# Optimization experiments

Hardware: AMD Instinct MI355X
Metric: run time of the kernel (lower is better)

Reference implementation:

```python
import jax, jax.numpy as jnp
import numpy as np

B, S, D = 2, 2048, 2048
H = 16
KV_RANK, Q_RANK = 512, 1536
NOPE, ROPE_D, VD = 128, 64, 128
QK_D = NOPE + ROPE_D  # 192


def _rope(t, positions):
    # t: (B, H, S, d) with d even; rotate-half RoPE, theta=10000
    d = t.shape[-1]
    inv_freq = 1.0 / (10000.0 ** (jnp.arange(0, d, 2, dtype=jnp.float32) / d))
    ang = positions.astype(jnp.float32)[:, None] * inv_freq  # (S, d//2)
    cos, sin = jnp.cos(ang), jnp.sin(ang)                    # (S, d//2)
    t1, t2 = t[..., : d // 2], t[..., d // 2 :]
    return jnp.concatenate([t1 * cos - t2 * sin, t2 * cos + t1 * sin], axis=-1)


def setup_inputs() -> dict:
    key = jax.random.key(0)
    ks = jax.random.split(key, 10)
    sc = 0.02
    return {
        "x": jax.random.normal(ks[0], (B, S, D), dtype=jnp.float32),
        "positions": jnp.arange(S, dtype=jnp.int32),
        # torch.nn.Linear weights are (out_features, in_features)
        "Wq_down": jax.random.normal(ks[1], (Q_RANK, D), dtype=jnp.float32) * sc,
        "Wq_up": jax.random.normal(ks[2], (H * NOPE, Q_RANK), dtype=jnp.float32) * sc,
        "Wq_rope": jax.random.normal(ks[3], (H * ROPE_D, Q_RANK), dtype=jnp.float32) * sc,
        "Wkv_down": jax.random.normal(ks[4], (KV_RANK, D), dtype=jnp.float32) * sc,
        "Wk_up": jax.random.normal(ks[5], (H * NOPE, KV_RANK), dtype=jnp.float32) * sc,
        "Wv_up": jax.random.normal(ks[6], (H * VD, KV_RANK), dtype=jnp.float32) * sc,
        "Wk_rope": jax.random.normal(ks[7], (ROPE_D, D), dtype=jnp.float32) * sc,
        "Wo": jax.random.normal(ks[8], (D, H * VD), dtype=jnp.float32) * sc,
    }


def reference(x, positions, Wq_down, Wq_up, Wq_rope, Wkv_down, Wk_up, Wv_up, Wk_rope, Wo):
    bsz, seq_len, _ = x.shape

    # Query path: low-rank down, then nope + rope up-projections
    c_q = x @ Wq_down.T                                             # (B, S, Q_RANK)
    q_c = (c_q @ Wq_up.T).reshape(bsz, seq_len, H, NOPE).transpose(0, 2, 1, 3)
    q_r = (c_q @ Wq_rope.T).reshape(bsz, seq_len, H, ROPE_D).transpose(0, 2, 1, 3)
    q_r = _rope(q_r, positions)
    q = jnp.concatenate([q_c, q_r], axis=-1)                        # (B, H, S, QK_D)

    # KV path: shared latent, single rope head broadcast to all heads
    c_kv = x @ Wkv_down.T                                           # (B, S, KV_RANK)
    k_c = (c_kv @ Wk_up.T).reshape(bsz, seq_len, H, NOPE).transpose(0, 2, 1, 3)
    v_c = (c_kv @ Wv_up.T).reshape(bsz, seq_len, H, VD).transpose(0, 2, 1, 3)
    k_r = (x @ Wk_rope.T).reshape(bsz, seq_len, 1, ROPE_D).transpose(0, 2, 1, 3)
    k_r = _rope(k_r, positions)
    k_r = jnp.broadcast_to(k_r, (bsz, H, seq_len, ROPE_D))
    k = jnp.concatenate([k_c, k_r], axis=-1)                        # (B, H, S, QK_D)

    # Causal SDPA, scale = 1/sqrt(total qk head dim)
    scale = 1.0 / math.sqrt(QK_D) if False else QK_D ** -0.5
    scores = jnp.einsum("bhqd,bhkd->bhqk", q, k) * scale
    causal = jnp.tril(jnp.ones((seq_len, seq_len), dtype=bool))
    scores = jnp.where(causal, scores, jnp.finfo(scores.dtype).min)
    attn = jax.nn.softmax(scores, axis=-1)
    out = jnp.einsum("bhqk,bhkd->bhqd", attn, v_c)                  # (B, H, S, VD)

    out = out.transpose(0, 2, 1, 3).reshape(bsz, seq_len, H * VD)
    return out @ Wo.T                                               # (B, S, D)
```

## Files before the change

### kernel.cpp

```cpp
#include <hip/hip_runtime.h>
#include <cmath>

#define SLEN 2048

typedef __bf16 bf16x8 __attribute__((ext_vector_type(8)));
typedef float  f32x4  __attribute__((ext_vector_type(4)));

__device__ inline void gld16(const void* g, void* l) {
    __builtin_amdgcn_global_load_lds(
        (const __attribute__((address_space(1))) void*)(uintptr_t)g,
        (__attribute__((address_space(3))) void*)(unsigned)(uintptr_t)l, 16, 0, 0);
}

struct CvArgs {
    const float* src[9];
    __bf16*      dst[9];
    long         cum[10];
};
__global__ __launch_bounds__(256)
void convert_all(CvArgs a) {
    long i8 = ((long)blockIdx.x * 256 + threadIdx.x) * 8;
    if (i8 >= a.cum[9]) return;
    int s = 0;
#pragma unroll
    for (int k = 1; k < 9; k++) if (i8 >= a.cum[k]) s = k;
    long loc = i8 - a.cum[s];
    const float* sp = a.src[s] + loc;
    float4 u0 = *(const float4*)(sp);
    float4 u1 = *(const float4*)(sp + 4);
    bf16x8 o;
    o[0] = (__bf16)u0.x; o[1] = (__bf16)u0.y; o[2] = (__bf16)u0.z; o[3] = (__bf16)u0.w;
    o[4] = (__bf16)u1.x; o[5] = (__bf16)u1.y; o[6] = (__bf16)u1.z; o[7] = (__bf16)u1.w;
    *(bf16x8*)(a.dst[s] + loc) = o;
}

struct Outs { __bf16* a; __bf16* b; __bf16* c; float* f; };

__global__ __launch_bounds__(256, 2)
void gemm_nt(const __bf16* __restrict__ A, const __bf16* __restrict__ B,
             Outs o, const int* __restrict__ positions,
             int M, int N, int K, int mode, float scale, int n_off) {
    __shared__ __bf16 As[128 * 64];
    __shared__ __bf16 Bs[128 * 64];
    int tid = threadIdx.x;
    int wave = tid >> 6, lane = tid & 63;
    int lane15 = lane & 15, quad = lane >> 4;
    int ri = lane >> 3, ci = lane & 7;
    int cg = ci ^ ri;
    int m0 = blockIdx.x * 128, n0 = blockIdx.y * 128 + n_off;
    int wm = (wave & 1) * 64, wn = (wave >> 1) * 64;
    f32x4 acc[4][4] = {};

    for (int k0 = 0; k0 < K; k0 += 64) {
#pragma unroll
        for (int t = 0; t < 4; t++) {
            int rr = wave * 32 + t * 8;
            int r = rr + ri;
            gld16(A + (size_t)(m0 + r) * K + k0 + cg * 8, As + rr * 64);
            int br = n0 + r; if (br > N - 1) br = N - 1;
            gld16(B + (size_t)br * K + k0 + cg * 8, Bs + rr * 64);
        }
        __syncthreads();
#pragma unroll
        for (int kk = 0; kk < 64; kk += 32) {
            int jb = kk >> 3;
            bf16x8 af[4], bfr[4];
#pragma unroll
            for (int mt = 0; mt < 4; mt++) {
                int rA = wm + mt * 16 + lane15;
                af[mt] = *(bf16x8*)(As + rA * 64 + (((jb + quad) ^ (rA & 7)) << 3));
            }
#pragma unroll
            for (int nt = 0; nt < 4; nt++) {
                int rB = wn + nt * 16 + lane15;
                bfr[nt] = *(bf16x8*)(Bs + rB * 64 + (((jb + quad) ^ (rB & 7)) << 3));
            }
#pragma unroll
            for (int mt = 0; mt < 4; mt++)
#pragma unroll
                for (int nt = 0; nt < 4; nt++)
                    acc[mt][nt] = __builtin_amdgcn_mfma_f32_16x16x32_bf16(
                        af[mt], bfr[nt], acc[mt][nt], 0, 0, 0);
        }
        __syncthreads();
    }

    const float KLOG = 13.287712379549449f / 32.0f;

    if (mode == 8 && n0 == 2048) {
        if (wn == 0) {
#pragma unroll
            for (int mt = 0; mt < 4; mt++) {
                int row = m0 + wm + mt * 16 + quad * 4;
#pragma unroll
                for (int nt = 0; nt < 2; nt++) {
                    int i = nt * 16 + lane15;
                    float inv = exp2f(-(float)i * KLOG);
#pragma unroll
                    for (int r = 0; r < 4; r++) {
                        int tok = row + r;
                        float p = (float)positions[tok & (SLEN - 1)];
                        float sn, cs; sincosf(p * inv, &sn, &cs);
                        float t1 = acc[mt][nt][r], t2 = acc[mt][nt + 2][r];
                        float rot1 = t1 * cs - t2 * sn;
                        float rot2 = t2 * cs + t1 * sn;
                        size_t ob = (size_t)tok * 3072 + 128;
#pragma unroll
                        for (int hh = 0; hh < 16; hh++) {
                            o.c[ob + hh * 192 + i]      = (__bf16)rot1;
                            o.c[ob + hh * 192 + 32 + i] = (__bf16)rot2;
                        }
                    }
                }
            }
        }
        return;
    }
}

__global__ __launch_bounds__(512, 2)
void gemm_nt2(const __bf16* __restrict__ A, const __bf16* __restrict__ B,
              Outs o, const int* __restrict__ positions,
              int N, int K, int mode, float scale) {
    __shared__ __bf16 As[2][256 * 64];
    __shared__ __bf16 Bs[2][128 * 64];
    int tid = threadIdx.x;
    int wave = tid >> 6, lane = tid & 63;
    int lane15 = lane & 15, quad = lane >> 4;
    int wr = wave >> 1, wc = wave & 1;
    int lr = lane >> 3, lc = lane & 7;

    int nblk = gridDim.x;
    int qq = nblk >> 3;
    int bid = blockIdx.x;
    int wg = (bid & 7) * qq + (bid >> 3);
    int m0 = (wg & 15) * 256;
    int n0 = (wg >> 4) * 128;

    f32x4 acc[4][4] = {};
    int NT = K >> 6;

    auto stageA = [&](int t, int k0, int buf) {
        int rr = t * 64 + wave * 8;
        int r = rr + lr;
        int cg = lc ^ (r & 7);
        gld16(A + (size_t)(m0 + r) * K + k0 + cg * 8, &As[buf][0] + rr * 64);
    };
    auto stageB = [&](int t, int k0, int buf) {
        int rr = t * 64 + wave * 8;
        int r = rr + lr;
        int cg = lc ^ (r & 7);
        int br = n0 + r; if (br > N - 1) br = N - 1;
        gld16(B + (size_t)br * K + k0 + cg * 8, &Bs[buf][0] + rr * 64);
    };

#pragma unroll
    for (int t = 0; t < 4; t++) stageA(t, 0, 0);
#pragma unroll
    for (int t = 0; t < 2; t++) stageB(t, 0, 0);
    __syncthreads();

    for (int t = 0; t < NT; t++) {
        int cur = t & 1;
        int k1 = (t + 1) << 6;
        bool more = (t + 1) < NT;

        if (more) { stageA(0, k1, cur ^ 1); stageA(1, k1, cur ^ 1); stageB(0, k1, cur ^ 1); }
        {
            bf16x8 af[4], bfr[4];
#pragma unroll
            for (int mt = 0; mt < 4; mt++) {
                int rA = wr * 64 + mt * 16 + lane15;
                af[mt] = *(bf16x8*)(&As[cur][0] + rA * 64 + ((quad ^ (rA & 7)) << 3));
            }
#pragma unroll
            for (int nt = 0; nt < 4; nt++) {
                int rB = wc * 64 + nt * 16 + lane15;
                bfr[nt] = *(bf16x8*)(&Bs[cur][0] + rB * 64 + ((quad ^ (rB & 7)) << 3));
            }
            __builtin_amdgcn_s_setprio(1);
#pragma unroll
            for (int mt = 0; mt < 4; mt++)
#pragma unroll
                for (int nt = 0; nt < 4; nt++)
                    acc[mt][nt] = __builtin_amdgcn_mfma_f32_16x16x32_bf16(
                        af[mt], bfr[nt], acc[mt][nt], 0, 0, 0);
            __builtin_amdgcn_s_setprio(0);
        }
        __builtin_amdgcn_s_barrier();

        if (more) { stageA(2, k1, cur ^ 1); stageA(3, k1, cur ^ 1); stageB(1, k1, cur ^ 1); }
        {
            bf16x8 af[4], bfr[4];
#pragma unroll
            for (int mt = 0; mt < 4; mt++) {
                int rA = wr * 64 + mt * 16 + lane15;
                af[mt] = *(bf16x8*)(&As[cur][0] + rA * 64 + (((4 + quad) ^ (rA & 7)) << 3));
            }
#pragma unroll
            for (int nt = 0; nt < 4; nt++) {
                int rB = wc * 64 + nt * 16 + lane15;
                bfr[nt] = *(bf16x8*)(&Bs[cur][0] + rB * 64 + (((4 + quad) ^ (rB & 7)) << 3));
            }
            __builtin_amdgcn_s_setprio(1);
#pragma unroll
            for (int mt = 0; mt < 4; mt++)
#pragma unroll
                for (int nt = 0; nt < 4; nt++)
                    acc[mt][nt] = __builtin_amdgcn_mfma_f32_16x16x32_bf16(
                        af[mt], bfr[nt], acc[mt][nt], 0, 0, 0);
            __builtin_amdgcn_s_setprio(0);
        }
        __syncthreads();
    }

    const float KLOG = 13.287712379549449f / 32.0f;

    if (mode == 9 && n0 >= 2048) {
        int hh = (n0 + wc * 64 - 2048) >> 6;
#pragma unroll
        for (int mt = 0; mt < 4; mt++) {
            int row = m0 + wr * 64 + mt * 16 + quad * 4;
#pragma unroll
            for (int nt = 0; nt < 2; nt++) {
                int i = nt * 16 + lane15;
                float inv = exp2f(-(float)i * KLOG);
#pragma unroll
                for (int r = 0; r < 4; r++) {
                    int tok = row + r;
                    float p = (float)positions[tok & (SLEN - 1)];
                    float sn, cs; sincosf(p * inv, &sn, &cs);
                    float t1 = acc[mt][nt][r], t2 = acc[mt][nt + 2][r];
                    size_t ob = (size_t)tok * 3072 + hh * 192 + 128;
                    o.a[ob + i]      = (__bf16)((t1 * cs - t2 * sn) * scale);
                    o.a[ob + 32 + i] = (__bf16)((t2 * cs + t1 * sn) * scale);
                }
            }
        }
        return;
    }

#pragma unroll
    for (int mt = 0; mt < 4; mt++) {
        int row = m0 + wr * 64 + mt * 16 + quad * 4;
#pragma unroll
        for (int nt = 0; nt < 4; nt++) {
            int col = n0 + wc * 64 + nt * 16 + lane15;
#pragma unroll
            for (int r = 0; r < 4; r++) {
                float v = acc[mt][nt][r];
                size_t rw = (size_t)(row + r);
                if (mode == 2) {
                    o.f[rw * N + col] = v;
                } else if (mode == 8) {
                    if (col < 1536) o.a[rw * 1536 + col] = (__bf16)v;
                    else            o.b[rw * 512 + col - 1536] = (__bf16)v;
                } else if (mode == 9) {
                    o.a[rw * 3072 + (col >> 7) * 192 + (col & 127)] =
                        (__bf16)(v * scale);
                } else {
                    if (col < 2048)
                        o.a[rw * 3072 + (col >> 7) * 192 + (col & 127)] = (__bf16)v;
                    else {
                        int d = col - 2048;
                        o.b[((size_t)d * 2 + (rw >> 11)) * 2048 + (rw & 2047)] = (__bf16)v;
                    }
                }
            }
        }
    }
}

__global__ __launch_bounds__(256, 2)
void mla_attn(const __bf16* __restrict__ Q, const __bf16* __restrict__ K,
              const __bf16* __restrict__ Vt, __bf16* __restrict__ O) {
    __shared__ __bf16 Ks[64 * 192];
    __shared__ __bf16 Vs[128 * 64];
    __shared__ __bf16 Ps[4][32][72];
    int tid = threadIdx.x, wave = tid >> 6, lane = tid & 63;
    int lane15 = lane & 15, quad = lane >> 4;
    int h = blockIdx.y, b = blockIdx.z;
    int x = blockIdx.x;
    int qt0 = (x & 1) ? (x >> 1) : (15 - (x >> 1));
    int qt = b ? (15 - qt0) : qt0;
    int q0 = qt * 128;
    const __bf16* Qb  = Q + (size_t)b * SLEN * 3072 + h * 192;
    const __bf16* Kb  = K + (size_t)b * SLEN * 3072 + h * 192;
    const __bf16* vtb = Vt + ((size_t)(h * 128) * 2 + b) * 2048;

    bf16x8 qf[2][6];
#pragma unroll
    for (int mt = 0; mt < 2; mt++) {
        int qrow = q0 + wave * 32 + mt * 16 + lane15;
#pragma unroll
        for (int kk = 0; kk < 6; kk++)
            qf[mt][kk] = *(const bf16x8*)(Qb + (size_t)qrow * 3072 + kk * 32 + quad * 8);
    }
    bf16x8 ones;
#pragma unroll
    for (int e = 0; e < 8; e++) ones[e] = (__bf16)1.0f;

    f32x4 o_acc[2][8] = {};
    float m_i[2][4], l_i[2][4];
#pragma unroll
    for (int mt = 0; mt < 2; mt++)
#pragma unroll
        for (int r = 0; r < 4; r++) { m_i[mt][r] = -3.0e38f; l_i[mt][r] = 0.0f; }

    for (int j0 = 0; j0 <= q0 + 64; j0 += 64) {
#pragma unroll
        for (int t = 0; t < 6; t++) {
            int sb = (wave * 6 + t) * 64;
            int slot = sb + lane;
            int r = slot / 24;
            int c = slot - r * 24;
            int cgk = (c & ~7) | ((c & 7) ^ (r & 7));
            gld16(Kb + (size_t)(j0 + r) * 3072 + cgk * 8, Ks + sb * 8);
        }
#pragma unroll
        for (int t = 0; t < 4; t++) {
            int sb = (wave * 4 + t) * 64;
            int slot = sb + lane;
            int r = slot >> 3, c = slot & 7;
            gld16(vtb + (size_t)r * 4096 + j0 + (c ^ (r & 7)) * 8, Vs + sb * 8);
        }
        __syncthreads();

        f32x4 acc[2][4] = {};
        __builtin_amdgcn_s_setprio(1);
#pragma unroll
        for (int kk = 0; kk < 6; kk++) {
#pragma unroll
            for (int nt = 0; nt < 4; nt++) {
                int n = nt * 16 + lane15;
                int j = kk * 4 + quad;
                int cl = (j & ~7) | ((j & 7) ^ (n & 7));
                bf16x8 kf = *(bf16x8*)(Ks + n * 192 + cl * 8);
#pragma unroll
                for (int mt = 0; mt < 2; mt++)
                    acc[mt][nt] = __builtin_amdgcn_mfma_f32_16x16x32_bf16(
                        qf[mt][kk], kf, acc[mt][nt], 0, 0, 0);
            }
        }
        __builtin_amdgcn_s_setprio(0);

        if (j0 >= q0) {
#pragma unroll
            for (int mt = 0; mt < 2; mt++) {
                int rowg = q0 + wave * 32 + mt * 16 + quad * 4;
#pragma unroll
                for (int nt = 0; nt < 4; nt++) {
                    int colg = j0 + nt * 16 + lane15;
#pragma unroll
                    for (int r = 0; r < 4; r++)
                        if (colg > rowg + r) acc[mt][nt][r] = -3.0e38f;
                }
            }
        }

        float mx[2][4];
        bool need = false;
#pragma unroll
        for (int mt = 0; mt < 2; mt++)
#pragma unroll
            for (int r = 0; r < 4; r++) {
                float v = fmaxf(fmaxf(acc[mt][0][r], acc[mt][1][r]),
                                fmaxf(acc[mt][2][r], acc[mt][3][r]));
                mx[mt][r] = v;
                need = need || (v > m_i[mt][r] + 24.0f);
            }
        if (__any(need)) {
#pragma unroll
            for (int mt = 0; mt < 2; mt++)
#pragma unroll
                for (int r = 0; r < 4; r++) {
                    float v = mx[mt][r];
#pragma unroll
                    for (int d = 8; d >= 1; d >>= 1) v = fmaxf(v, __shfl_xor(v, d));
                    float mn = fmaxf(m_i[mt][r], v);
                    float alpha = exp2f(m_i[mt][r] - mn);
                    m_i[mt][r] = mn;
                    l_i[mt][r] *= alpha;
#pragma unroll
                    for (int nt = 0; nt < 8; nt++) o_acc[mt][nt][r] *= alpha;
                }
        }

#pragma unroll
        for (int mt = 0; mt < 2; mt++)
#pragma unroll
            for (int r = 0; r < 4; r++)
#pragma unroll
                for (int nt = 0; nt < 4; nt++) {
                    float pp = exp2f(acc[mt][nt][r] - m_i[mt][r]);
                    Ps[wave][mt * 16 + quad * 4 + r][nt * 16 + lane15] = (__bf16)pp;
                }

        f32x4 rs[2] = {};
        __builtin_amdgcn_s_setprio(1);
#pragma unroll
        for (int ks = 0; ks < 2; ks++) {
            bf16x8 pf[2];
#pragma unroll
            for (int mt = 0; mt < 2; mt++)
                pf[mt] = *(bf16x8*)(&Ps[wave][mt * 16 + lane15][ks * 32 + quad * 8]);
#pragma unroll
            for (int nt = 0; nt < 8; nt++) {
                int nn = nt * 16 + lane15;
                int j = ks * 4 + quad;
                bf16x8 vf = *(bf16x8*)(Vs + nn * 64 + (j ^ (nn & 7)) * 8);
#pragma unroll
                for (int mt = 0; mt < 2; mt++)
                    o_acc[mt][nt] = __builtin_amdgcn_mfma_f32_16x16x32_bf16(
                        pf[mt], vf, o_acc[mt][nt], 0, 0, 0);
            }
#pragma unroll
            for (int mt = 0; mt < 2; mt++)
                rs[mt] = __builtin_amdgcn_mfma_f32_16x16x32_bf16(
                    pf[mt], ones, rs[mt], 0, 0, 0);
        }
        __builtin_amdgcn_s_setprio(0);
#pragma unroll
        for (int mt = 0; mt < 2; mt++)
#pragma unroll
            for (int r = 0; r < 4; r++) l_i[mt][r] += rs[mt][r];
        __syncthreads();
    }

    int tokb = b * SLEN + q0 + wave * 32 + quad * 4;
#pragma unroll
    for (int mt = 0; mt < 2; mt++) {
#pragma unroll
        for (int r = 0; r < 4; r++) {
            float inv_l = 1.0f / l_i[mt][r];
            int tok = tokb + mt * 16 + r;
#pragma unroll
            for (int nt = 0; nt < 8; nt++) {
                O[(size_t)tok * 2048 + h * 128 + nt * 16 + lane15] =
                    (__bf16)(o_acc[mt][nt][r] * inv_l);
            }
        }
    }
}

extern "C" void kernel_launch(void* const* d_in, const int* in_sizes, int n_in,
                              void* d_out, int out_size, void* d_ws, size_t ws_size,
                              hipStream_t stream) {
    (void)in_sizes; (void)n_in; (void)out_size; (void)ws_size;
    const int* pos = (const int*)d_in[1];
    float* out = (float*)d_out;

    char* ws = (char*)d_ws;
    size_t off = 0;
    auto alloc = [&](size_t bytes) {
        char* p = ws + off;
        off += (bytes + 255) & ~(size_t)255;
        return p;
    };
    __bf16* x_bf  = (__bf16*)alloc(8388608ull * 2);
    __bf16* Wcat1 = (__bf16*)alloc(4325376ull * 2);
    __bf16* Wcat2 = (__bf16*)alloc(4718592ull * 2);
    __bf16* Wcat3 = (__bf16*)alloc(4194304ull * 2);
    __bf16* Wob   = (__bf16*)alloc(4194304ull * 2);
    __bf16* c_q   = (__bf16*)alloc(4096ull * 1536 * 2);
    __bf16* c_kv  = (__bf16*)alloc(4096ull * 512 * 2);
    __bf16* v_t   = (__bf16*)alloc(4096ull * 2048 * 2);
    __bf16* q_all = (__bf16*)alloc(4096ull * 3072 * 2);
    __bf16* k_all = (__bf16*)alloc(4096ull * 3072 * 2);
    __bf16* attn_o = (__bf16*)c_q;

    const float scale_l2 = 1.4426950408889634f / sqrtf(192.0f);
    dim3 blk(256);
    dim3 blk2(512);

    CvArgs cv;
    cv.src[0] = (const float*)d_in[0]; cv.dst[0] = x_bf;
    cv.src[1] = (const float*)d_in[2]; cv.dst[1] = Wcat1;
    cv.src[2] = (const float*)d_in[5]; cv.dst[2] = Wcat1 + 3145728;
    cv.src[3] = (const float*)d_in[8]; cv.dst[3] = Wcat1 + 4194304;
    cv.src[4] = (const float*)d_in[3]; cv.dst[4] = Wcat2;
    cv.src[5] = (const float*)d_in[4]; cv.dst[5] = Wcat2 + 3145728;
    cv.src[6] = (const float*)d_in[6]; cv.dst[6] = Wcat3;
    cv.src[7] = (const float*)d_in[7]; cv.dst[7] = Wcat3 + 1048576;
    cv.src[8] = (const float*)d_in[9]; cv.dst[8] = Wob;
    long ns[9] = {8388608, 3145728, 1048576, 131072, 3145728, 1572864,
                  1048576, 1048576, 4194304};
    cv.cum[0] = 0;
    for (int i = 0; i < 9; i++) cv.cum[i + 1] = cv.cum[i] + ns[i];
    convert_all<<<dim3((unsigned)(cv.cum[9] / 2048)), blk, 0, stream>>>(cv);

    Outs o1 = { c_q, c_kv, nullptr, nullptr };
    gemm_nt2<<<dim3(256), blk2, 0, stream>>>(x_bf, Wcat1, o1, pos, 2048, 2048, 8, 1.0f);
    Outs o1b = { nullptr, nullptr, k_all, nullptr };
    gemm_nt<<<dim3(32, 1), blk, 0, stream>>>(x_bf, Wcat1, o1b, pos, 4096, 2112, 2048, 8, 1.0f, 2048);
    Outs o2 = { q_all, nullptr, nullptr, nullptr };
    gemm_nt2<<<dim3(384), blk2, 0, stream>>>(c_q, Wcat2, o2, pos, 3072, 1536, 9, scale_l2);
    Outs o3 = { k_all, v_t, nullptr, nullptr };
    gemm_nt2<<<dim3(512), blk2, 0, stream>>>(c_kv, Wcat3, o3, pos, 4096, 512, 10, 1.0f);
    mla_attn<<<dim3(16, 16, 2), blk, 0, stream>>>(q_all, k_all, v_t, attn_o);
    Outs o4 = { nullptr, nullptr, nullptr, out };
    gemm_nt2<<<dim3(256), blk2, 0, stream>>>(attn_o, Wob, o4, pos, 2048, 2048, 2, 1.0f);
}
```

Before: 479.4 us.

## Triple-buffer 128x256 GEMM, merge first projection, XCD-aware attention block mapping

Replaces the double-buffered 256x128 GEMM with a 128x256-tile kernel that uses three LDS stages, prefetches two k-steps ahead, and waits with explicit vmcnt/lgkmcnt barriers. The first projection now runs as a single gemm_nt launch covering all 2112 columns, replacing one large and one small launch, with occupancy raised to 3. The attention grid is remapped so that heads are spread across XCDs. Together these aim to hide global-load latency and improve cache locality, at the cost of more LDS per block and fragile hand-written wait counts.

New measurement: 457.5 us. 1.05x faster.

```diff
diff --git a/kernel.cpp b/kernel.cpp
--- a/kernel.cpp
+++ b/kernel.cpp
@@ -36,10 +36,10 @@
 
 struct Outs { __bf16* a; __bf16* b; __bf16* c; float* f; };
 
-__global__ __launch_bounds__(256, 2)
+__global__ __launch_bounds__(256, 3)
 void gemm_nt(const __bf16* __restrict__ A, const __bf16* __restrict__ B,
              Outs o, const int* __restrict__ positions,
-             int M, int N, int K, int mode, float scale, int n_off) {
+             int M, int N, int K, int mode, float scale) {
     __shared__ __bf16 As[128 * 64];
     __shared__ __bf16 Bs[128 * 64];
     int tid = threadIdx.x;
@@ -47,7 +47,7 @@
     int lane15 = lane & 15, quad = lane >> 4;
     int ri = lane >> 3, ci = lane & 7;
     int cg = ci ^ ri;
-    int m0 = blockIdx.x * 128, n0 = blockIdx.y * 128 + n_off;
+    int m0 = blockIdx.x * 128, n0 = blockIdx.y * 128;
     int wm = (wave & 1) * 64, wn = (wave >> 1) * 64;
     f32x4 acc[4][4] = {};
 
@@ -116,56 +116,78 @@
         }
         return;
     }
+
+#pragma unroll
+    for (int mt = 0; mt < 4; mt++) {
+        int row = m0 + wm + mt * 16 + quad * 4;
+#pragma unroll
+        for (int nt = 0; nt < 4; nt++) {
+            int col = n0 + wn + nt * 16 + lane15;
+            if (col < N) {
+#pragma unroll
+                for (int r = 0; r < 4; r++) {
+                    float v = acc[mt][nt][r];
+                    size_t rw = (size_t)(row + r);
+                    if (mode == 8) {
+                        if (col < 1536) o.a[rw * 1536 + col] = (__bf16)v;
+                        else            o.b[rw * 512 + col - 1536] = (__bf16)v;
+                    }
+                }
+            }
+        }
+    }
 }
 
 __global__ __launch_bounds__(512, 2)
-void gemm_nt2(const __bf16* __restrict__ A, const __bf16* __restrict__ B,
-              Outs o, const int* __restrict__ positions,
-              int N, int K, int mode, float scale) {
-    __shared__ __bf16 As[2][256 * 64];
-    __shared__ __bf16 Bs[2][128 * 64];
+void gemm8p(const __bf16* __restrict__ A, const __bf16* __restrict__ B,
+            Outs o, const int* __restrict__ positions,
+            int N, int K, int mode, float scale) {
+    __shared__ __bf16 As[3][128 * 64];
+    __shared__ __bf16 Bs[3][256 * 64];
     int tid = threadIdx.x;
     int wave = tid >> 6, lane = tid & 63;
     int lane15 = lane & 15, quad = lane >> 4;
-    int wr = wave >> 1, wc = wave & 1;
-    int lr = lane >> 3, lc = lane & 7;
-
-    int nblk = gridDim.x;
-    int qq = nblk >> 3;
+    int wr = wave >> 2, wc = wave & 3;
+
+    int nwg = gridDim.x;
+    int chnk = nwg >> 3;
     int bid = blockIdx.x;
-    int wg = (bid & 7) * qq + (bid >> 3);
-    int m0 = (wg & 15) * 256;
-    int n0 = (wg >> 4) * 128;
+    int wg = (bid & 7) * chnk + (bid >> 3);
+    int m0 = (wg & 31) * 128;
+    int n0 = (wg >> 5) * 256;
 
     f32x4 acc[4][4] = {};
     int NT = K >> 6;
 
-    auto stageA = [&](int t, int k0, int buf) {
-        int rr = t * 64 + wave * 8;
-        int r = rr + lr;
-        int cg = lc ^ (r & 7);
-        gld16(A + (size_t)(m0 + r) * K + k0 + cg * 8, &As[buf][0] + rr * 64);
+    auto stageA = [&](int kt, int buf) {
+#pragma unroll
+        for (int u = 0; u < 2; u++) {
+            int slot = u * 512 + wave * 64 + lane;
+            int r = slot >> 3, c = slot & 7;
+            gld16(A + (size_t)(m0 + r) * K + kt * 64 + ((c ^ (r & 7)) << 3),
+                  &As[buf][0] + (size_t)(u * 512 + wave * 64) * 8);
+        }
     };
-    auto stageB = [&](int t, int k0, int buf) {
-        int rr = t * 64 + wave * 8;
-        int r = rr + lr;
-        int cg = lc ^ (r & 7);
-        int br = n0 + r; if (br > N - 1) br = N - 1;
-        gld16(B + (size_t)br * K + k0 + cg * 8, &Bs[buf][0] + rr * 64);
+    auto stageBh = [&](int kt, int buf, int h) {
+#pragma unroll
+        for (int u = 0; u < 2; u++) {
+            int slot = (h * 2 + u) * 512 + wave * 64 + lane;
+            int r = slot >> 3, c = slot & 7;
+            gld16(B + (size_t)(n0 + r) * K + kt * 64 + ((c ^ (r & 7)) << 3),
+                  &Bs[buf][0] + (size_t)((h * 2 + u) * 512 + wave * 64) * 8);
+        }
     };
 
-#pragma unroll
-    for (int t = 0; t < 4; t++) stageA(t, 0, 0);
-#pragma unroll
-    for (int t = 0; t < 2; t++) stageB(t, 0, 0);
-    __syncthreads();
+    stageA(0, 0); stageBh(0, 0, 0); stageBh(0, 0, 1);
+    stageA(1, 1); stageBh(1, 1, 0); stageBh(1, 1, 1);
+    asm volatile("s_waitcnt vmcnt(6)" ::: "memory");
+    __builtin_amdgcn_s_barrier();
 
     for (int t = 0; t < NT; t++) {
-        int cur = t & 1;
-        int k1 = (t + 1) << 6;
-        bool more = (t + 1) < NT;
-
-        if (more) { stageA(0, k1, cur ^ 1); stageA(1, k1, cur ^ 1); stageB(0, k1, cur ^ 1); }
+        int cur = t % 3;
+        int pre = (t + 2) % 3;
+        bool more = (t + 2) < NT;
+
         {
             bf16x8 af[4], bfr[4];
 #pragma unroll
@@ -178,6 +200,10 @@
                 int rB = wc * 64 + nt * 16 + lane15;
                 bfr[nt] = *(bf16x8*)(&Bs[cur][0] + rB * 64 + ((quad ^ (rB & 7)) << 3));
             }
+            if (more) { stageA(t + 2, pre); stageBh(t + 2, pre, 0); }
+            __builtin_amdgcn_s_barrier();
+            asm volatile("s_waitcnt lgkmcnt(0)" ::: "memory");
+            __builtin_amdgcn_sched_barrier(0);
             __builtin_amdgcn_s_setprio(1);
 #pragma unroll
             for (int mt = 0; mt < 4; mt++)
@@ -186,10 +212,9 @@
                     acc[mt][nt] = __builtin_amdgcn_mfma_f32_16x16x32_bf16(
                         af[mt], bfr[nt], acc[mt][nt], 0, 0, 0);
             __builtin_amdgcn_s_setprio(0);
-        }
-        __builtin_amdgcn_s_barrier();
-
-        if (more) { stageA(2, k1, cur ^ 1); stageA(3, k1, cur ^ 1); stageB(1, k1, cur ^ 1); }
+            __builtin_amdgcn_s_barrier();
+        }
+
         {
             bf16x8 af[4], bfr[4];
 #pragma unroll
@@ -202,6 +227,10 @@
                 int rB = wc * 64 + nt * 16 + lane15;
                 bfr[nt] = *(bf16x8*)(&Bs[cur][0] + rB * 64 + (((4 + quad) ^ (rB & 7)) << 3));
             }
+            if (more) stageBh(t + 2, pre, 1);
+            __builtin_amdgcn_s_barrier();
+            asm volatile("s_waitcnt lgkmcnt(0)" ::: "memory");
+            __builtin_amdgcn_sched_barrier(0);
             __builtin_amdgcn_s_setprio(1);
 #pragma unroll
             for (int mt = 0; mt < 4; mt++)
@@ -210,8 +239,12 @@
                     acc[mt][nt] = __builtin_amdgcn_mfma_f32_16x16x32_bf16(
                         af[mt], bfr[nt], acc[mt][nt], 0, 0, 0);
             __builtin_amdgcn_s_setprio(0);
-        }
-        __syncthreads();
+            if (t + 1 < NT) {
+                if (more) asm volatile("s_waitcnt vmcnt(6)" ::: "memory");
+                else      asm volatile("s_waitcnt vmcnt(0)" ::: "memory");
+            }
+            __builtin_amdgcn_s_barrier();
+        }
     }
 
     const float KLOG = 13.287712379549449f / 32.0f;
@@ -252,9 +285,6 @@
                 size_t rw = (size_t)(row + r);
                 if (mode == 2) {
                     o.f[rw * N + col] = v;
-                } else if (mode == 8) {
-                    if (col < 1536) o.a[rw * 1536 + col] = (__bf16)v;
-                    else            o.b[rw * 512 + col - 1536] = (__bf16)v;
                 } else if (mode == 9) {
                     o.a[rw * 3072 + (col >> 7) * 192 + (col & 127)] =
                         (__bf16)(v * scale);
@@ -279,8 +309,13 @@
     __shared__ __bf16 Ps[4][32][72];
     int tid = threadIdx.x, wave = tid >> 6, lane = tid & 63;
     int lane15 = lane & 15, quad = lane >> 4;
-    int h = blockIdx.y, b = blockIdx.z;
-    int x = blockIdx.x;
+
+    int lin = blockIdx.x + (blockIdx.y << 4) + (blockIdx.z << 8);
+    int xcd = lin & 7, slot = lin >> 3;
+    int x = slot & 15;
+    int g = xcd + ((slot >> 4) << 3);
+    int h = g & 15, b = g >> 4;
+
     int qt0 = (x & 1) ? (x >> 1) : (15 - (x >> 1));
     int qt = b ? (15 - qt0) : qt0;
     int q0 = qt * 128;
@@ -311,17 +346,17 @@
 #pragma unroll
         for (int t = 0; t < 6; t++) {
             int sb = (wave * 6 + t) * 64;
-            int slot = sb + lane;
-            int r = slot / 24;
-            int c = slot - r * 24;
+            int slot2 = sb + lane;
+            int r = slot2 / 24;
+            int c = slot2 - r * 24;
             int cgk = (c & ~7) | ((c & 7) ^ (r & 7));
             gld16(Kb + (size_t)(j0 + r) * 3072 + cgk * 8, Ks + sb * 8);
         }
 #pragma unroll
         for (int t = 0; t < 4; t++) {
             int sb = (wave * 4 + t) * 64;
-            int slot = sb + lane;
-            int r = slot >> 3, c = slot & 7;
+            int slot2 = sb + lane;
+            int r = slot2 >> 3, c = slot2 & 7;
             gld16(vtb + (size_t)r * 4096 + j0 + (c ^ (r & 7)) * 8, Vs + sb * 8);
         }
         __syncthreads();
@@ -471,7 +506,7 @@
 
     const float scale_l2 = 1.4426950408889634f / sqrtf(192.0f);
     dim3 blk(256);
-    dim3 blk2(512);
+    dim3 blk8(512);
 
     CvArgs cv;
     cv.src[0] = (const float*)d_in[0]; cv.dst[0] = x_bf;
@@ -489,15 +524,13 @@
     for (int i = 0; i < 9; i++) cv.cum[i + 1] = cv.cum[i] + ns[i];
     convert_all<<<dim3((unsigned)(cv.cum[9] / 2048)), blk, 0, stream>>>(cv);
 
-    Outs o1 = { c_q, c_kv, nullptr, nullptr };
-    gemm_nt2<<<dim3(256), blk2, 0, stream>>>(x_bf, Wcat1, o1, pos, 2048, 2048, 8, 1.0f);
-    Outs o1b = { nullptr, nullptr, k_all, nullptr };
-    gemm_nt<<<dim3(32, 1), blk, 0, stream>>>(x_bf, Wcat1, o1b, pos, 4096, 2112, 2048, 8, 1.0f, 2048);
+    Outs o1 = { c_q, c_kv, k_all, nullptr };
+    gemm_nt<<<dim3(32, 17), blk, 0, stream>>>(x_bf, Wcat1, o1, pos, 4096, 2112, 2048, 8, 1.0f);
     Outs o2 = { q_all, nullptr, nullptr, nullptr };
-    gemm_nt2<<<dim3(384), blk2, 0, stream>>>(c_q, Wcat2, o2, pos, 3072, 1536, 9, scale_l2);
+    gemm8p<<<dim3(384), blk8, 0, stream>>>(c_q, Wcat2, o2, pos, 3072, 1536, 9, scale_l2);
     Outs o3 = { k_all, v_t, nullptr, nullptr };
-    gemm_nt2<<<dim3(512), blk2, 0, stream>>>(c_kv, Wcat3, o3, pos, 4096, 512, 10, 1.0f);
+    gemm8p<<<dim3(512), blk8, 0, stream>>>(c_kv, Wcat3, o3, pos, 4096, 512, 10, 1.0f);
     mla_attn<<<dim3(16, 16, 2), blk, 0, stream>>>(q_all, k_all, v_t, attn_o);
     Outs o4 = { nullptr, nullptr, nullptr, out };
-    gemm_nt2<<<dim3(256), blk2, 0, stream>>>(attn_o, Wob, o4, pos, 2048, 2048, 2, 1.0f);
+    gemm8p<<<dim3(256), blk8, 0, stream>>>(attn_o, Wob, o4, pos, 2048, 2048, 2, 1.0f);
 }
```
